# Optimization experiments

Measured on AMD Instinct MI355X. Metric: run time of the kernel, lower is better.

Reference implementation:

```python
import jax, jax.numpy as jnp
import numpy as np


def setup_inputs() -> dict:
    key = jax.random.key(0)
    k1, k2 = jax.random.split(key)
    B, C, D = 8192, 8192, 256
    x = jax.random.normal(k1, (B, D), dtype=jnp.float32)
    y = jax.random.normal(k2, (C, D), dtype=jnp.float32)
    gamma = jnp.ones((), dtype=jnp.float32)
    return {"x": x, "y": y, "gamma": gamma}


def reference(x, y, gamma):
    # RBF kernel: exp(-gamma * ||x_i - y_j||^2), shape (B, C).
    # avoiding the O(B*C*D) broadcast-diff intermediate of the naive form.
    x2 = jnp.sum(x * x, axis=-1)          # (B,)
    y2 = jnp.sum(y * y, axis=-1)          # (C,)
    xy = jnp.einsum('bd,cd->bc', x, y)    # (B, C) GEMM
    sq_dist = x2[:, None] + y2[None, :] - 2.0 * xy
    sq_dist = jnp.maximum(sq_dist, 0.0)   # guard tiny negatives from cancellation
    return jnp.exp(-gamma * sq_dist)
```

## Files before the change

kernel.cpp:

```cpp
#include <hip/hip_runtime.h>
#include <hip/hip_bf16.h>

typedef __bf16 bf16_t;
typedef __attribute__((ext_vector_type(8))) __bf16 bf16x8;
typedef __attribute__((ext_vector_type(4))) __bf16 bf16x4;
typedef __attribute__((ext_vector_type(4))) float floatx4;

#define NB 8192
#define NC 8192
#define ND 256
#define BM 128
#define BN 128
#define BK 64
#define LOG2E 1.44269504088896340736f

typedef __attribute__((address_space(3))) void lds_void_t;
typedef __attribute__((address_space(1))) void gl_void_t;

__global__ __launch_bounds__(256) void prep_kernel(
    const float* __restrict__ x, const float* __restrict__ y,
    const float* __restrict__ gamma_p,
    bf16_t* __restrict__ xb, bf16_t* __restrict__ yb,
    float* __restrict__ x2s, float* __restrict__ y2s)
{
    int t    = threadIdx.x;
    int wave = t >> 6;
    int lane = t & 63;
    int row  = blockIdx.x * 4 + wave;

    const float* src;
    bf16_t* dst;
    float* nrm;
    int r;
    if (row < NB) { src = x; dst = xb; nrm = x2s; r = row; }
    else          { src = y; dst = yb; nrm = y2s; r = row - NB; }

    float4 v = ((const float4*)(src + (size_t)r * ND))[lane];
    float ss = v.x * v.x + v.y * v.y + v.z * v.z + v.w * v.w;

    bf16x4 o;
    o.x = (__bf16)v.x; o.y = (__bf16)v.y; o.z = (__bf16)v.z; o.w = (__bf16)v.w;
    ((bf16x4*)(dst + (size_t)r * ND))[lane] = o;

    #pragma unroll
    for (int off = 32; off >= 1; off >>= 1)
        ss += __shfl_xor(ss, off, 64);
    if (lane == 0) nrm[r] = ss * (LOG2E * gamma_p[0]);
}

__global__ __launch_bounds__(256, 3) void rbf_gemm_kernel(
    const bf16_t* __restrict__ xb, const bf16_t* __restrict__ yb,
    const float* __restrict__ x2s, const float* __restrict__ y2s,
    const float* __restrict__ gamma_p, float* __restrict__ out)
{
    __shared__ bf16_t lA[BM * BK];
    __shared__ bf16_t lB[BN * BK];

    const int t    = threadIdx.x;
    const int lane = t & 63;
    const int wave = t >> 6;
    const int wm   = wave >> 1;
    const int wn   = wave & 1;
    const int quad = lane >> 4;
    const int l15  = lane & 15;

    const int bm = blockIdx.x * BM;
    const int bn = blockIdx.y * BN;

    const float A2 = 2.0f * LOG2E * gamma_p[0];

    floatx4 acc[4][4];
    #pragma unroll
    for (int i = 0; i < 4; ++i)
        #pragma unroll
        for (int j = 0; j < 4; ++j)
            acc[i][j] = (floatx4){0.f, 0.f, 0.f, 0.f};

    const char* gA = (const char*)xb + (size_t)bm * (ND * 2);
    const char* gB = (const char*)yb + (size_t)bn * (ND * 2);

    for (int kt = 0; kt < ND / BK; ++kt) {
        __syncthreads();
        #pragma unroll
        for (int c = 0; c < 4; ++c) {
            const int li  = c * 256 + t;
            const int row = li >> 3;
            const int kb  = (li & 7) * 16;
            const int kbs = kb ^ ((row & 7) << 4);
            const size_t goff = (size_t)row * (ND * 2) + kt * (BK * 2) + kbs;
            __builtin_amdgcn_global_load_lds(
                (gl_void_t*)(gA + goff),
                (lds_void_t*)((char*)lA + (size_t)li * 16), 16, 0, 0);
            __builtin_amdgcn_global_load_lds(
                (gl_void_t*)(gB + goff),
                (lds_void_t*)((char*)lB + (size_t)li * 16), 16, 0, 0);
        }
        __syncthreads();

        #pragma unroll
        for (int kk = 0; kk < 2; ++kk) {
            bf16x8 af[4], bfr[4];
            const int swz = ((l15 & 7) << 4);
            const int off = (kk * 64 + quad * 16) ^ swz;
            #pragma unroll
            for (int i = 0; i < 4; ++i) {
                const int ar = wm * 64 + i * 16 + l15;
                af[i]  = *(const bf16x8*)((const char*)lA + ar * (BK * 2) + off);
                const int br = wn * 64 + i * 16 + l15;
                bfr[i] = *(const bf16x8*)((const char*)lB + br * (BK * 2) + off);
            }
            #pragma unroll
            for (int i = 0; i < 4; ++i)
                #pragma unroll
                for (int j = 0; j < 4; ++j)
                    acc[i][j] = __builtin_amdgcn_mfma_f32_16x16x32_bf16(
                        af[i], bfr[j], acc[i][j], 0, 0, 0);
        }
    }

    #pragma unroll
    for (int i = 0; i < 4; ++i) {
        const int grow0 = bm + wm * 64 + i * 16 + quad * 4;
        float xn[4];
        #pragma unroll
        for (int r = 0; r < 4; ++r) xn[r] = x2s[grow0 + r];
        #pragma unroll
        for (int j = 0; j < 4; ++j) {
            const int gcol = bn + wn * 64 + j * 16 + l15;
            const float yn = y2s[gcol];
            #pragma unroll
            for (int r = 0; r < 4; ++r) {
                float t2 = fmaf(A2, acc[i][j][r], -(xn[r] + yn));
                t2 = fminf(t2, 0.0f);
                out[(size_t)(grow0 + r) * NC + gcol] = exp2f(t2);
            }
        }
    }
}

extern "C" void kernel_launch(void* const* d_in, const int* in_sizes, int n_in,
                              void* d_out, int out_size, void* d_ws, size_t ws_size,
                              hipStream_t stream) {
    const float* x = (const float*)d_in[0];
    const float* y = (const float*)d_in[1];
    const float* gamma = (const float*)d_in[2];
    float* out = (float*)d_out;

    bf16_t* xb = (bf16_t*)d_ws;
    bf16_t* yb = xb + (size_t)NB * ND;
    float*  x2s = (float*)(yb + (size_t)NC * ND);
    float*  y2s = x2s + NB;

    prep_kernel<<<dim3((NB + NC) / 4), dim3(256), 0, stream>>>(
        x, y, gamma, xb, yb, x2s, y2s);
    rbf_gemm_kernel<<<dim3(NB / BM, NC / BN), dim3(256), 0, stream>>>(
        xb, yb, x2s, y2s, gamma, out);
}
```

Before: 289.4 us.

## Load GEMM operands directly from global, remap tiles per XCD, nontemporal stores

Drops the LDS staging and barriers of the GEMM. Each wave now loads its bf16 fragments straight from global memory, relying on L2 because K is only 256. Adds an XCD-aware block-index remap so the blocks on each XCD share A/B tiles in their local L2. Switches the output writes to nontemporal stores so the 256MB output does not pollute the cache. The risk is redundant global and L1 traffic, since each row is now fetched by two waves, and loads with less coalescing than the staged path.

```diff
diff --git a/kernel.cpp b/kernel.cpp
--- a/kernel.cpp
+++ b/kernel.cpp
@@ -11,11 +11,7 @@
 #define ND 256
 #define BM 128
 #define BN 128
-#define BK 64
 #define LOG2E 1.44269504088896340736f
-
-typedef __attribute__((address_space(3))) void lds_void_t;
-typedef __attribute__((address_space(1))) void gl_void_t;
 
 __global__ __launch_bounds__(256) void prep_kernel(
     const float* __restrict__ x, const float* __restrict__ y,
@@ -53,9 +49,6 @@
     const float* __restrict__ x2s, const float* __restrict__ y2s,
     const float* __restrict__ gamma_p, float* __restrict__ out)
 {
-    __shared__ bf16_t lA[BM * BK];
-    __shared__ bf16_t lB[BN * BK];
-
     const int t    = threadIdx.x;
     const int lane = t & 63;
     const int wave = t >> 6;
@@ -64,10 +57,26 @@
     const int quad = lane >> 4;
     const int l15  = lane & 15;
 
-    const int bm = blockIdx.x * BM;
-    const int bn = blockIdx.y * BN;
+    const unsigned n   = blockIdx.y * 64u + blockIdx.x;
+    const unsigned xcd = n & 7u;
+    const unsigned s   = n >> 3;
+    const unsigned tbm = (xcd & 1u) * 32u + (s & 31u);
+    const unsigned tbn = (xcd >> 1) * 16u + (s >> 5);
+
+    const int bm = (int)tbm * BM;
+    const int bn = (int)tbn * BN;
 
     const float A2 = 2.0f * LOG2E * gamma_p[0];
+
+    const char* abase[4];
+    const char* bbase[4];
+    #pragma unroll
+    for (int i = 0; i < 4; ++i) {
+        abase[i] = (const char*)xb
+                 + (size_t)(bm + wm * 64 + i * 16 + l15) * (ND * 2) + quad * 16;
+        bbase[i] = (const char*)yb
+                 + (size_t)(bn + wn * 64 + i * 16 + l15) * (ND * 2) + quad * 16;
+    }
 
     floatx4 acc[4][4];
     #pragma unroll
@@ -76,38 +85,16 @@
         for (int j = 0; j < 4; ++j)
             acc[i][j] = (floatx4){0.f, 0.f, 0.f, 0.f};
 
-    const char* gA = (const char*)xb + (size_t)bm * (ND * 2);
-    const char* gB = (const char*)yb + (size_t)bn * (ND * 2);
-
-    for (int kt = 0; kt < ND / BK; ++kt) {
-        __syncthreads();
-        #pragma unroll
-        for (int c = 0; c < 4; ++c) {
-            const int li  = c * 256 + t;
-            const int row = li >> 3;
-            const int kb  = (li & 7) * 16;
-            const int kbs = kb ^ ((row & 7) << 4);
-            const size_t goff = (size_t)row * (ND * 2) + kt * (BK * 2) + kbs;
-            __builtin_amdgcn_global_load_lds(
-                (gl_void_t*)(gA + goff),
-                (lds_void_t*)((char*)lA + (size_t)li * 16), 16, 0, 0);
-            __builtin_amdgcn_global_load_lds(
-                (gl_void_t*)(gB + goff),
-                (lds_void_t*)((char*)lB + (size_t)li * 16), 16, 0, 0);
-        }
-        __syncthreads();
-
+    #pragma unroll
+    for (int kt = 0; kt < 4; ++kt) {
         #pragma unroll
         for (int kk = 0; kk < 2; ++kk) {
+            const int off = kt * 128 + kk * 64;
             bf16x8 af[4], bfr[4];
-            const int swz = ((l15 & 7) << 4);
-            const int off = (kk * 64 + quad * 16) ^ swz;
             #pragma unroll
             for (int i = 0; i < 4; ++i) {
-                const int ar = wm * 64 + i * 16 + l15;
-                af[i]  = *(const bf16x8*)((const char*)lA + ar * (BK * 2) + off);
-                const int br = wn * 64 + i * 16 + l15;
-                bfr[i] = *(const bf16x8*)((const char*)lB + br * (BK * 2) + off);
+                af[i]  = *(const bf16x8*)(abase[i] + off);
+                bfr[i] = *(const bf16x8*)(bbase[i] + off);
             }
             #pragma unroll
             for (int i = 0; i < 4; ++i)
@@ -132,7 +119,8 @@
             for (int r = 0; r < 4; ++r) {
                 float t2 = fmaf(A2, acc[i][j][r], -(xn[r] + yn));
                 t2 = fminf(t2, 0.0f);
-                out[(size_t)(grow0 + r) * NC + gcol] = exp2f(t2);
+                __builtin_nontemporal_store(
+                    exp2f(t2), out + (size_t)(grow0 + r) * NC + gcol);
             }
         }
     }
```

Result: slower. 378.4 us (+30.7%).

## Double-buffer LDS tiles with BK=32 to overlap global loads with MFMA

Applied to the files above, without the earlier changes.

Splits the K loop into 32-wide tiles held in two LDS buffers, so the next tile is prefetched with global_load_lds while MFMAs run on the current one. This drops one barrier per iteration and keeps LDS usage the same. The swizzle is reduced to 4 rows to match the narrower tile. In exchange there are twice as many K iterations, and the kernel likely stays bound by the output store (a 256 MB fp32 write).

```diff
diff --git a/kernel.cpp b/kernel.cpp
--- a/kernel.cpp
+++ b/kernel.cpp
@@ -11,7 +11,7 @@
 #define ND 256
 #define BM 128
 #define BN 128
-#define BK 64
+#define BK 32
 #define LOG2E 1.44269504088896340736f
 
 typedef __attribute__((address_space(3))) void lds_void_t;
@@ -53,8 +53,8 @@
     const float* __restrict__ x2s, const float* __restrict__ y2s,
     const float* __restrict__ gamma_p, float* __restrict__ out)
 {
-    __shared__ bf16_t lA[BM * BK];
-    __shared__ bf16_t lB[BN * BK];
+    __shared__ bf16_t lA[2][BM * BK];
+    __shared__ bf16_t lB[2][BN * BK];
 
     const int t    = threadIdx.x;
     const int lane = t & 63;
@@ -79,44 +79,54 @@
     const char* gA = (const char*)xb + (size_t)bm * (ND * 2);
     const char* gB = (const char*)yb + (size_t)bn * (ND * 2);
 
+    #define STAGE(dbuf, ktile)                                                 \
+        do {                                                                   \
+            _Pragma("unroll")                                                  \
+            for (int c = 0; c < 2; ++c) {                                      \
+                const int li  = c * 256 + t;                                   \
+                const int row = li >> 2;                                       \
+                const int kb  = (li & 3) * 16;                                 \
+                const int kbs = kb ^ ((row & 3) << 4);                         \
+                const size_t goff =                                            \
+                    (size_t)row * (ND * 2) + (ktile) * (BK * 2) + kbs;         \
+                __builtin_amdgcn_global_load_lds(                              \
+                    (gl_void_t*)(gA + goff),                                   \
+                    (lds_void_t*)((char*)&lA[dbuf][0] + (size_t)li * 16),      \
+                    16, 0, 0);                                                 \
+                __builtin_amdgcn_global_load_lds(                              \
+                    (gl_void_t*)(gB + goff),                                   \
+                    (lds_void_t*)((char*)&lB[dbuf][0] + (size_t)li * 16),      \
+                    16, 0, 0);                                                 \
+            }                                                                  \
+        } while (0)
+
+    STAGE(0, 0);
+    __syncthreads();
+
     for (int kt = 0; kt < ND / BK; ++kt) {
+        const int cur = kt & 1;
+        if (kt < ND / BK - 1)
+            STAGE(cur ^ 1, kt + 1);
+
+        bf16x8 af[4], bfr[4];
+        const int off = (quad * 16) ^ ((l15 & 3) << 4);
+        #pragma unroll
+        for (int i = 0; i < 4; ++i) {
+            const int ar = wm * 64 + i * 16 + l15;
+            af[i]  = *(const bf16x8*)((const char*)&lA[cur][0] + ar * (BK * 2) + off);
+            const int br = wn * 64 + i * 16 + l15;
+            bfr[i] = *(const bf16x8*)((const char*)&lB[cur][0] + br * (BK * 2) + off);
+        }
+        #pragma unroll
+        for (int i = 0; i < 4; ++i)
+            #pragma unroll
+            for (int j = 0; j < 4; ++j)
+                acc[i][j] = __builtin_amdgcn_mfma_f32_16x16x32_bf16(
+                    af[i], bfr[j], acc[i][j], 0, 0, 0);
+
         __syncthreads();
-        #pragma unroll
-        for (int c = 0; c < 4; ++c) {
-            const int li  = c * 256 + t;
-            const int row = li >> 3;
-            const int kb  = (li & 7) * 16;
-            const int kbs = kb ^ ((row & 7) << 4);
-            const size_t goff = (size_t)row * (ND * 2) + kt * (BK * 2) + kbs;
-            __builtin_amdgcn_global_load_lds(
-                (gl_void_t*)(gA + goff),
-                (lds_void_t*)((char*)lA + (size_t)li * 16), 16, 0, 0);
-            __builtin_amdgcn_global_load_lds(
-                (gl_void_t*)(gB + goff),
-                (lds_void_t*)((char*)lB + (size_t)li * 16), 16, 0, 0);
-        }
-        __syncthreads();
-
-        #pragma unroll
-        for (int kk = 0; kk < 2; ++kk) {
-            bf16x8 af[4], bfr[4];
-            const int swz = ((l15 & 7) << 4);
-            const int off = (kk * 64 + quad * 16) ^ swz;
-            #pragma unroll
-            for (int i = 0; i < 4; ++i) {
-                const int ar = wm * 64 + i * 16 + l15;
-                af[i]  = *(const bf16x8*)((const char*)lA + ar * (BK * 2) + off);
-                const int br = wn * 64 + i * 16 + l15;
-                bfr[i] = *(const bf16x8*)((const char*)lB + br * (BK * 2) + off);
-            }
-            #pragma unroll
-            for (int i = 0; i < 4; ++i)
-                #pragma unroll
-                for (int j = 0; j < 4; ++j)
-                    acc[i][j] = __builtin_amdgcn_mfma_f32_16x16x32_bf16(
-                        af[i], bfr[j], acc[i][j], 0, 0, 0);
-        }
     }
+    #undef STAGE
 
     #pragma unroll
     for (int i = 0; i < 4; ++i) {
```

Result: slower. 302.6 us (+4.5%).
